# Kernel optimization log

Hardware: AMD Instinct MI355X
Metric: run time of the kernel (lower is better)

Reference implementation:

```python
import jax, jax.numpy as jnp
import numpy as np

WORLD_SIZE = 8
RANK = 3              # simulated rank; exercises a non-trivial zig-zag mask
Q_HEAD = 32
KV_HEAD = 8
HEAD_DIM = 128
SEQLEN = 8192                         # max_seqlen_q == max_seqlen_k
Q_SHARD_LEN = SEQLEN // WORLD_SIZE    # 1024 tokens per rank
CHUNK = Q_SHARD_LEN // 2              # zig-zag chunk size (512)
GROUP = Q_HEAD // KV_HEAD             # GQA group size


def _zigzag_pos(r):
    # Global token positions owned by rank r under zig-zag partitioning:
    # sequence split into 2W chunks; rank r owns chunks r and (2W-1-r).
    a = jnp.arange(CHUNK) + r * CHUNK
    b = jnp.arange(CHUNK) + (2 * WORLD_SIZE - 1 - r) * CHUNK
    return jnp.concatenate([a, b])


def setup_inputs() -> dict:
    key = jax.random.key(0)
    k1, k2, k3 = jax.random.split(key, 3)
    q_shard = jax.random.normal(k1, (Q_SHARD_LEN, Q_HEAD, HEAD_DIM), jnp.float32)
    k_shard = jax.random.normal(k2, (WORLD_SIZE, SEQLEN // WORLD_SIZE, KV_HEAD, HEAD_DIM), jnp.float32)
    v_shard = jax.random.normal(k3, (WORLD_SIZE, SEQLEN // WORLD_SIZE, KV_HEAD, HEAD_DIM), jnp.float32)
    cu_seqlens_q = jnp.array([0, Q_SHARD_LEN], dtype=jnp.int32)
    cu_seqlens_k = jnp.array([0, SEQLEN], dtype=jnp.int32)
    return {"q_shard": q_shard, "k_shard": k_shard, "v_shard": v_shard,
            "cu_seqlens_q": cu_seqlens_q, "cu_seqlens_k": cu_seqlens_k}


def reference(q_shard, k_shard, v_shard, cu_seqlens_q, cu_seqlens_k):
    # All-gather of k/v shards across ranks == concat along sequence axis.
    k = k_shard.reshape(SEQLEN, KV_HEAD, HEAD_DIM)
    v = v_shard.reshape(SEQLEN, KV_HEAD, HEAD_DIM)

    # Global positions for this rank's queries and the gathered keys
    q_pos = _zigzag_pos(RANK)                                               # [Lq]
    k_pos = jnp.concatenate([_zigzag_pos(r) for r in range(WORLD_SIZE)])    # [Sk]

    scale = 1.0 / np.sqrt(HEAD_DIM).astype(np.float32)
    qg = q_shard.reshape(Q_SHARD_LEN, KV_HEAD, GROUP, HEAD_DIM)
    # scores: [Hkv, G, Lq, Sk]
    scores = jnp.einsum('qhgd,khd->hgqk', qg, k) * scale

    # Zig-zag causal mask on GLOBAL positions
    causal = q_pos[:, None] >= k_pos[None, :]                               # [Lq, Sk]
    scores = jnp.where(causal[None, None], scores, -jnp.inf)

    p = jax.nn.softmax(scores, axis=-1)
    out = jnp.einsum('hgqk,khd->qhgd', p, v)
    return out.reshape(Q_SHARD_LEN, Q_HEAD, HEAD_DIM)
```

## Files before the change

### kernel.cpp

```cpp
#include <hip/hip_runtime.h>
#include <hip/hip_bf16.h>

typedef __bf16 bf16x8 __attribute__((ext_vector_type(8)));
typedef float  f32x4  __attribute__((ext_vector_type(4)));

#define LQ   1024
#define HQ   32
#define HKV  8
#define GRP  4
#define DH   128
#define CHK  512
#define KB   32
#define RHN  (LQ * HQ)
#define NSPLIT 4
#define QSCALE (0.08838834764831845f * 1.44269504088896341f)
#define MASKVAL (-3.0e38f)


__device__ __forceinline__ void attn_tile(
    char* __restrict__ lds, char* __restrict__ pbase,
    const float* __restrict__ kg, const float* __restrict__ vg,
    int hkv, int krow, int cbase, bool masked,
    int tid, int l16, int lhi, int qrel0,
    const bf16x8 (&qf)[4], f32x4 (&acc)[8], float (&m_r)[4], float (&l_r)[4])
{
    __syncthreads();
    {
        const int key = tid >> 3;
        const int d0  = (tid & 7) << 4;
        const float* kp = kg + ((krow + key) * HKV + hkv) * DH + d0;
        const float* vp = vg + ((krow + key) * HKV + hkv) * DH + d0;
        f32x4 a0 = *(const f32x4*)(kp);
        f32x4 a1 = *(const f32x4*)(kp + 4);
        f32x4 a2 = *(const f32x4*)(kp + 8);
        f32x4 a3 = *(const f32x4*)(kp + 12);
        bf16x8 b0, b1;
        #pragma unroll
        for (int j = 0; j < 4; ++j) {
            b0[j] = (__bf16)a0[j]; b0[j + 4] = (__bf16)a1[j];
            b1[j] = (__bf16)a2[j]; b1[j + 4] = (__bf16)a3[j];
        }
        const int kbyte = key * 256 + d0 * 2;
        const int ksw   = (key & 7) << 4;
        *(bf16x8*)(lds + ((kbyte)      ^ ksw)) = b0;
        *(bf16x8*)(lds + ((kbyte + 16) ^ ksw)) = b1;

        f32x4 c0 = *(const f32x4*)(vp);
        f32x4 c1 = *(const f32x4*)(vp + 4);
        f32x4 c2 = *(const f32x4*)(vp + 8);
        f32x4 c3 = *(const f32x4*)(vp + 12);
        #pragma unroll
        for (int i = 0; i < 16; ++i) {
            float fv = (i < 4) ? c0[i] : (i < 8) ? c1[i - 4]
                     : (i < 12) ? c2[i - 8] : c3[i - 12];
            const int d = d0 + i;
            const int vsw = ((d & 7) ^ ((d >> 4) & 7)) << 4;
            const int vbyte = (d * 64 + key * 2) ^ vsw;
            *(__bf16*)(lds + 8192 + vbyte) = (__bf16)fv;
        }
    }
    __syncthreads();

    f32x4 s0 = f32x4{0.f, 0.f, 0.f, 0.f};
    f32x4 s1 = f32x4{0.f, 0.f, 0.f, 0.f};
    __builtin_amdgcn_s_setprio(1);
    #pragma unroll
    for (int kb = 0; kb < 4; ++kb) {
        const int dby = (kb * 32 + lhi * 8) * 2;
        bf16x8 k0 = *(const bf16x8*)(lds + ((l16 * 256 + dby)        ^ ((l16 & 7) << 4)));
        bf16x8 k1 = *(const bf16x8*)(lds + (((l16 + 16) * 256 + dby) ^ ((l16 & 7) << 4)));
        s0 = __builtin_amdgcn_mfma_f32_16x16x32_bf16(qf[kb], k0, s0, 0, 0, 0);
        s1 = __builtin_amdgcn_mfma_f32_16x16x32_bf16(qf[kb], k1, s1, 0, 0, 0);
    }
    __builtin_amdgcn_s_setprio(0);

    if (masked) {
        #pragma unroll
        for (int r = 0; r < 4; ++r) {
            const int qrel = qrel0 + lhi * 4 + r;
            if (cbase + l16 > qrel)      s0[r] = MASKVAL;
            if (cbase + 16 + l16 > qrel) s1[r] = MASKVAL;
        }
    }

    float pmax[4];
    #pragma unroll
    for (int r = 0; r < 4; ++r) pmax[r] = fmaxf(s0[r], s1[r]);
    #pragma unroll
    for (int off = 1; off < 16; off <<= 1) {
        #pragma unroll
        for (int r = 0; r < 4; ++r)
            pmax[r] = fmaxf(pmax[r], __shfl_xor(pmax[r], off));
    }

    f32x4 p0, p1;
    float alpha[4], rsum[4];
    #pragma unroll
    for (int r = 0; r < 4; ++r) {
        const float mnew = fmaxf(m_r[r], pmax[r]);
        alpha[r] = exp2f(m_r[r] - mnew);
        m_r[r]   = mnew;
        p0[r] = exp2f(s0[r] - mnew);
        p1[r] = exp2f(s1[r] - mnew);
        rsum[r] = p0[r] + p1[r];
    }
    #pragma unroll
    for (int off = 1; off < 16; off <<= 1) {
        #pragma unroll
        for (int r = 0; r < 4; ++r)
            rsum[r] += __shfl_xor(rsum[r], off);
    }
    #pragma unroll
    for (int r = 0; r < 4; ++r) l_r[r] = l_r[r] * alpha[r] + rsum[r];
    #pragma unroll
    for (int nb = 0; nb < 8; ++nb) {
        #pragma unroll
        for (int r = 0; r < 4; ++r) acc[nb][r] *= alpha[r];
    }

    #pragma unroll
    for (int r = 0; r < 4; ++r) {
        const int rq  = lhi * 4 + r;
        const int rsw = (rq & 7) << 4;
        *(__bf16*)(pbase + ((rq * 64 + l16 * 2)        ^ rsw)) = (__bf16)p0[r];
        *(__bf16*)(pbase + ((rq * 64 + (l16 + 16) * 2) ^ rsw)) = (__bf16)p1[r];
    }
    bf16x8 pa = *(const bf16x8*)(pbase + ((l16 * 64 + lhi * 16) ^ ((l16 & 7) << 4)));
    __builtin_amdgcn_s_setprio(1);
    #pragma unroll
    for (int nb = 0; nb < 8; ++nb) {
        const int d = nb * 16 + l16;
        const int vsw = ((d & 7) ^ (nb & 7)) << 4;
        bf16x8 vb = *(const bf16x8*)(lds + 8192 + ((d * 64 + lhi * 16) ^ vsw));
        acc[nb] = __builtin_amdgcn_mfma_f32_16x16x32_bf16(pa, vb, acc[nb], 0, 0, 0);
    }
    __builtin_amdgcn_s_setprio(0);
}

__device__ __forceinline__ void load_qfrag(const float* __restrict__ qg,
                                           int qr0, int h, int l16, int lhi,
                                           bf16x8 (&qf)[4])
{
    const float* qp = qg + ((qr0 + l16) * HQ + h) * DH + lhi * 8;
    #pragma unroll
    for (int kb = 0; kb < 4; ++kb) {
        f32x4 t0 = *(const f32x4*)(qp + kb * 32);
        f32x4 t1 = *(const f32x4*)(qp + kb * 32 + 4);
        bf16x8 f;
        #pragma unroll
        for (int j = 0; j < 4; ++j) {
            f[j]     = (__bf16)(t0[j] * QSCALE);
            f[j + 4] = (__bf16)(t1[j] * QSCALE);
        }
        qf[kb] = f;
    }
}

__global__ __launch_bounds__(256, 2)
void zz_attn_part(const float* __restrict__ qg, const float* __restrict__ kg,
                  const float* __restrict__ vg,
                  float* __restrict__ Op, float* __restrict__ mp, float* __restrict__ lp)
{
    __shared__ __align__(16) char lds[20480];
    const int bid = blockIdx.x;
    int half, part, q_tile, hkv;
    if (bid < 256) { half = 0; part = 0; q_tile = bid & 31;              hkv = bid >> 5; }
    else { const int e = bid - 256; half = 1; part = e & 3;
           q_tile = 32 + ((e >> 2) & 31);                                hkv = e >> 7; }

    const int tid  = threadIdx.x;
    const int w    = tid >> 6;
    const int lane = tid & 63;
    const int l16  = lane & 15;
    const int lhi  = lane >> 4;
    const int h    = hkv * GRP + w;
    const int qr0  = q_tile << 4;
    const int qrel0 = (q_tile & 31) << 4;

    bf16x8 qf[4];
    load_qfrag(qg, qr0, h, l16, lhi, qf);

    f32x4 acc[8];
    #pragma unroll
    for (int i = 0; i < 8; ++i) acc[i] = f32x4{0.f, 0.f, 0.f, 0.f};
    float m_r[4], l_r[4];
    #pragma unroll
    for (int r = 0; r < 4; ++r) { m_r[r] = -1e30f; l_r[r] = 0.f; }

    char* const pbase = lds + 16384 + w * 1024;

    unsigned fullmask;
    int diag_slot;
    if (half == 0) { fullmask = 0x0015u; diag_slot = 6; }
    else {
        fullmask = (part == 0) ? 0x0015u : (part == 1) ? 0x0340u
                 : (part == 2) ? 0x1C00u : 0xE000u;
        diag_slot = (part == 3) ? 7 : -1;
    }

    #pragma unroll 1
    for (int s = 0; s < 16; ++s) {
        if (!((fullmask >> s) & 1)) continue;
        #pragma unroll 1
        for (int t = 0; t < 16; ++t)
            attn_tile(lds, pbase, kg, vg, hkv, s * CHK + t * KB, 0, false,
                      tid, l16, lhi, qrel0, qf, acc, m_r, l_r);
    }
    if (diag_slot >= 0) {
        const int nd = (qrel0 >> 5) + 1;
        #pragma unroll 1
        for (int t = 0; t < nd; ++t)
            attn_tile(lds, pbase, kg, vg, hkv, diag_slot * CHK + t * KB, t * KB, true,
                      tid, l16, lhi, qrel0, qf, acc, m_r, l_r);
    }

    float* op = Op + (size_t)part * (LQ * HQ * DH) + ((qr0 + lhi * 4) * HQ + h) * DH + l16;
    #pragma unroll
    for (int nb = 0; nb < 8; ++nb) {
        #pragma unroll
        for (int r = 0; r < 4; ++r)
            op[r * (HQ * DH) + nb * 16] = acc[nb][r];
    }
    if (l16 == 0) {
        #pragma unroll
        for (int r = 0; r < 4; ++r) {
            const int rh = (qr0 + lhi * 4 + r) * HQ + h;
            mp[part * RHN + rh] = m_r[r];
            lp[part * RHN + rh] = l_r[r];
            if (half == 0) {
                #pragma unroll
                for (int s = 1; s < NSPLIT; ++s) {
                    mp[s * RHN + rh] = -1e30f;
                    lp[s * RHN + rh] = 0.f;
                }
            }
        }
    }
}

__global__ __launch_bounds__(256)
void zz_combine(const float* __restrict__ Op, const float* __restrict__ mp,
                const float* __restrict__ lp, float* __restrict__ outg)
{
    const int flat = blockIdx.x * 256 + threadIdx.x;
    const int rh = flat >> 5;
    const int d4 = (flat & 31) << 2;
    const float m0 = mp[rh], m1 = mp[RHN + rh], m2 = mp[2 * RHN + rh], m3 = mp[3 * RHN + rh];
    const float M  = fmaxf(fmaxf(m0, m1), fmaxf(m2, m3));
    const float w0 = exp2f(m0 - M), w1 = exp2f(m1 - M), w2 = exp2f(m2 - M), w3 = exp2f(m3 - M);
    const float den = w0 * lp[rh] + w1 * lp[RHN + rh] + w2 * lp[2 * RHN + rh] + w3 * lp[3 * RHN + rh];
    const size_t base = (size_t)rh * DH + d4;
    f32x4 a0 = *(const f32x4*)(Op + base);
    f32x4 a1 = *(const f32x4*)(Op + (size_t)LQ * HQ * DH + base);
    f32x4 a2 = *(const f32x4*)(Op + (size_t)2 * LQ * HQ * DH + base);
    f32x4 a3 = *(const f32x4*)(Op + (size_t)3 * LQ * HQ * DH + base);
    f32x4 num = w0 * a0 + w1 * a1 + w2 * a2 + w3 * a3;
    const float inv = 1.0f / den;
    *(f32x4*)(outg + base) = num * inv;
}

__global__ __launch_bounds__(256, 2)
void zz_attn_mono(const float* __restrict__ qg, const float* __restrict__ kg,
                  const float* __restrict__ vg, float* __restrict__ outg)
{
    __shared__ __align__(16) char lds[20480];
    const int bid    = blockIdx.x;
    const int q_tile = bid & 63;
    const int hkv    = bid >> 6;
    const int tid    = threadIdx.x;
    const int w      = tid >> 6;
    const int lane   = tid & 63;
    const int l16    = lane & 15;
    const int lhi    = lane >> 4;
    const int h      = hkv * GRP + w;
    const int qr0    = q_tile << 4;
    const int half   = q_tile >> 5;
    const int qrel0  = (q_tile & 31) << 4;

    bf16x8 qf[4];
    load_qfrag(qg, qr0, h, l16, lhi, qf);

    f32x4 acc[8];
    #pragma unroll
    for (int i = 0; i < 8; ++i) acc[i] = f32x4{0.f, 0.f, 0.f, 0.f};
    float m_r[4], l_r[4];
    #pragma unroll
    for (int r = 0; r < 4; ++r) { m_r[r] = -1e30f; l_r[r] = 0.f; }

    char* const pbase = lds + 16384 + w * 1024;

    const unsigned int fullmask = half ? 0xFF55u : 0x0015u;
    const int diag_slot = half ? 7 : 6;

    #pragma unroll 1
    for (int s = 0; s < 16; ++s) {
        if (!((fullmask >> s) & 1)) continue;
        #pragma unroll 1
        for (int t = 0; t < 16; ++t)
            attn_tile(lds, pbase, kg, vg, hkv, s * CHK + t * KB, 0, false,
                      tid, l16, lhi, qrel0, qf, acc, m_r, l_r);
    }
    const int nd = (qrel0 >> 5) + 1;
    #pragma unroll 1
    for (int t = 0; t < nd; ++t)
        attn_tile(lds, pbase, kg, vg, hkv, diag_slot * CHK + t * KB, t * KB, true,
                  tid, l16, lhi, qrel0, qf, acc, m_r, l_r);

    #pragma unroll
    for (int r = 0; r < 4; ++r) l_r[r] = 1.0f / l_r[r];
    float* op = outg + (qr0 + lhi * 4) * (HQ * DH) + h * DH + l16;
    #pragma unroll
    for (int nb = 0; nb < 8; ++nb) {
        #pragma unroll
        for (int r = 0; r < 4; ++r)
            op[r * (HQ * DH) + nb * 16] = acc[nb][r] * l_r[r];
    }
}

extern "C" void kernel_launch(void* const* d_in, const int* in_sizes, int n_in,
                              void* d_out, int out_size, void* d_ws, size_t ws_size,
                              hipStream_t stream)
{
    (void)in_sizes; (void)n_in; (void)out_size;
    const float* q = (const float*)d_in[0];
    const float* k = (const float*)d_in[1];
    const float* v = (const float*)d_in[2];
    float* out = (float*)d_out;

    const size_t need = (size_t)NSPLIT * LQ * HQ * DH * 4
                      + (size_t)2 * NSPLIT * RHN * 4;
    if (ws_size >= need) {
        float* Op = (float*)d_ws;
        float* mp = Op + (size_t)NSPLIT * LQ * HQ * DH;
        float* lp = mp + (size_t)NSPLIT * RHN;
        hipLaunchKernelGGL(zz_attn_part, dim3(1280), dim3(256), 0, stream, q, k, v, Op, mp, lp);
        hipLaunchKernelGGL(zz_combine, dim3((RHN * DH / 4) / 256), dim3(256), 0, stream,
                           Op, mp, lp, out);
    } else {
        hipLaunchKernelGGL(zz_attn_mono, dim3(512), dim3(256), 0, stream, q, k, v, out);
    }
}
```

Baseline: 448.9 us.

## Pre-convert K/V to bf16 tiles and double-buffer with async global-to-LDS loads

Adds a prep kernel that converts K and V once into bf16, pre-swizzled and pre-transposed tiles in workspace. The main kernel then streams those tiles straight into a double-buffered LDS with global_load_lds, so the next tile loads while the current one computes, and it drops the per-tile fp32-to-bf16 conversion and scattered V stores. It also reorders the block index so heads are interleaved and raises occupancy to 4 blocks per CU. The cost is an extra kernel launch, an extra pass over K/V memory, and more LDS per block. The fallback path now also requires the split workspace.

```diff
diff --git a/kernel.cpp b/kernel.cpp
--- a/kernel.cpp
+++ b/kernel.cpp
@@ -13,129 +13,14 @@
 #define KB   32
 #define RHN  (LQ * HQ)
 #define NSPLIT 4
+#define TILE_BYTES 8192
+#define HKV_BYTES  (256 * TILE_BYTES)
 #define QSCALE (0.08838834764831845f * 1.44269504088896341f)
 #define MASKVAL (-3.0e38f)
 
-
-__device__ __forceinline__ void attn_tile(
-    char* __restrict__ lds, char* __restrict__ pbase,
-    const float* __restrict__ kg, const float* __restrict__ vg,
-    int hkv, int krow, int cbase, bool masked,
-    int tid, int l16, int lhi, int qrel0,
-    const bf16x8 (&qf)[4], f32x4 (&acc)[8], float (&m_r)[4], float (&l_r)[4])
-{
-    __syncthreads();
-    {
-        const int key = tid >> 3;
-        const int d0  = (tid & 7) << 4;
-        const float* kp = kg + ((krow + key) * HKV + hkv) * DH + d0;
-        const float* vp = vg + ((krow + key) * HKV + hkv) * DH + d0;
-        f32x4 a0 = *(const f32x4*)(kp);
-        f32x4 a1 = *(const f32x4*)(kp + 4);
-        f32x4 a2 = *(const f32x4*)(kp + 8);
-        f32x4 a3 = *(const f32x4*)(kp + 12);
-        bf16x8 b0, b1;
-        #pragma unroll
-        for (int j = 0; j < 4; ++j) {
-            b0[j] = (__bf16)a0[j]; b0[j + 4] = (__bf16)a1[j];
-            b1[j] = (__bf16)a2[j]; b1[j + 4] = (__bf16)a3[j];
-        }
-        const int kbyte = key * 256 + d0 * 2;
-        const int ksw   = (key & 7) << 4;
-        *(bf16x8*)(lds + ((kbyte)      ^ ksw)) = b0;
-        *(bf16x8*)(lds + ((kbyte + 16) ^ ksw)) = b1;
-
-        f32x4 c0 = *(const f32x4*)(vp);
-        f32x4 c1 = *(const f32x4*)(vp + 4);
-        f32x4 c2 = *(const f32x4*)(vp + 8);
-        f32x4 c3 = *(const f32x4*)(vp + 12);
-        #pragma unroll
-        for (int i = 0; i < 16; ++i) {
-            float fv = (i < 4) ? c0[i] : (i < 8) ? c1[i - 4]
-                     : (i < 12) ? c2[i - 8] : c3[i - 12];
-            const int d = d0 + i;
-            const int vsw = ((d & 7) ^ ((d >> 4) & 7)) << 4;
-            const int vbyte = (d * 64 + key * 2) ^ vsw;
-            *(__bf16*)(lds + 8192 + vbyte) = (__bf16)fv;
-        }
-    }
-    __syncthreads();
-
-    f32x4 s0 = f32x4{0.f, 0.f, 0.f, 0.f};
-    f32x4 s1 = f32x4{0.f, 0.f, 0.f, 0.f};
-    __builtin_amdgcn_s_setprio(1);
-    #pragma unroll
-    for (int kb = 0; kb < 4; ++kb) {
-        const int dby = (kb * 32 + lhi * 8) * 2;
-        bf16x8 k0 = *(const bf16x8*)(lds + ((l16 * 256 + dby)        ^ ((l16 & 7) << 4)));
-        bf16x8 k1 = *(const bf16x8*)(lds + (((l16 + 16) * 256 + dby) ^ ((l16 & 7) << 4)));
-        s0 = __builtin_amdgcn_mfma_f32_16x16x32_bf16(qf[kb], k0, s0, 0, 0, 0);
-        s1 = __builtin_amdgcn_mfma_f32_16x16x32_bf16(qf[kb], k1, s1, 0, 0, 0);
-    }
-    __builtin_amdgcn_s_setprio(0);
-
-    if (masked) {
-        #pragma unroll
-        for (int r = 0; r < 4; ++r) {
-            const int qrel = qrel0 + lhi * 4 + r;
-            if (cbase + l16 > qrel)      s0[r] = MASKVAL;
-            if (cbase + 16 + l16 > qrel) s1[r] = MASKVAL;
-        }
-    }
-
-    float pmax[4];
-    #pragma unroll
-    for (int r = 0; r < 4; ++r) pmax[r] = fmaxf(s0[r], s1[r]);
-    #pragma unroll
-    for (int off = 1; off < 16; off <<= 1) {
-        #pragma unroll
-        for (int r = 0; r < 4; ++r)
-            pmax[r] = fmaxf(pmax[r], __shfl_xor(pmax[r], off));
-    }
-
-    f32x4 p0, p1;
-    float alpha[4], rsum[4];
-    #pragma unroll
-    for (int r = 0; r < 4; ++r) {
-        const float mnew = fmaxf(m_r[r], pmax[r]);
-        alpha[r] = exp2f(m_r[r] - mnew);
-        m_r[r]   = mnew;
-        p0[r] = exp2f(s0[r] - mnew);
-        p1[r] = exp2f(s1[r] - mnew);
-        rsum[r] = p0[r] + p1[r];
-    }
-    #pragma unroll
-    for (int off = 1; off < 16; off <<= 1) {
-        #pragma unroll
-        for (int r = 0; r < 4; ++r)
-            rsum[r] += __shfl_xor(rsum[r], off);
-    }
-    #pragma unroll
-    for (int r = 0; r < 4; ++r) l_r[r] = l_r[r] * alpha[r] + rsum[r];
-    #pragma unroll
-    for (int nb = 0; nb < 8; ++nb) {
-        #pragma unroll
-        for (int r = 0; r < 4; ++r) acc[nb][r] *= alpha[r];
-    }
-
-    #pragma unroll
-    for (int r = 0; r < 4; ++r) {
-        const int rq  = lhi * 4 + r;
-        const int rsw = (rq & 7) << 4;
-        *(__bf16*)(pbase + ((rq * 64 + l16 * 2)        ^ rsw)) = (__bf16)p0[r];
-        *(__bf16*)(pbase + ((rq * 64 + (l16 + 16) * 2) ^ rsw)) = (__bf16)p1[r];
-    }
-    bf16x8 pa = *(const bf16x8*)(pbase + ((l16 * 64 + lhi * 16) ^ ((l16 & 7) << 4)));
-    __builtin_amdgcn_s_setprio(1);
-    #pragma unroll
-    for (int nb = 0; nb < 8; ++nb) {
-        const int d = nb * 16 + l16;
-        const int vsw = ((d & 7) ^ (nb & 7)) << 4;
-        bf16x8 vb = *(const bf16x8*)(lds + 8192 + ((d * 64 + lhi * 16) ^ vsw));
-        acc[nb] = __builtin_amdgcn_mfma_f32_16x16x32_bf16(pa, vb, acc[nb], 0, 0, 0);
-    }
-    __builtin_amdgcn_s_setprio(0);
-}
+typedef __attribute__((address_space(1))) const void gvoid_t;
+typedef __attribute__((address_space(3))) void lvoid_t;
+#define GLL(g, l) __builtin_amdgcn_global_load_lds((gvoid_t*)(g), (lvoid_t*)(l), 16, 0, 0)
 
 __device__ __forceinline__ void load_qfrag(const float* __restrict__ qg,
                                            int qr0, int h, int l16, int lhi,
@@ -156,17 +41,55 @@
     }
 }
 
-__global__ __launch_bounds__(256, 2)
-void zz_attn_part(const float* __restrict__ qg, const float* __restrict__ kg,
-                  const float* __restrict__ vg,
-                  float* __restrict__ Op, float* __restrict__ mp, float* __restrict__ lp)
-{
-    __shared__ __align__(16) char lds[20480];
+__global__ __launch_bounds__(256)
+void zz_prep(const float* __restrict__ kg, const float* __restrict__ vg,
+             char* __restrict__ Kp, char* __restrict__ Vp)
+{
+    const int bid  = blockIdx.x;
+    const int hkv  = bid & 7;
+    const int tile = bid >> 3;
+    const int tid  = threadIdx.x;
+    char* ko = Kp + (size_t)hkv * HKV_BYTES + (size_t)tile * TILE_BYTES;
+    char* vo = Vp + (size_t)hkv * HKV_BYTES + (size_t)tile * TILE_BYTES;
+
+    #pragma unroll
+    for (int p = 0; p < 2; ++p) {
+        const int gid = tid + p * 256;
+        const int key = gid >> 4;
+        const int dbg = gid & 15;
+        const float* src = kg + ((size_t)(tile * 32 + key) * HKV + hkv) * DH + dbg * 8;
+        f32x4 t0 = *(const f32x4*)src;
+        f32x4 t1 = *(const f32x4*)(src + 4);
+        bf16x8 b;
+        #pragma unroll
+        for (int j = 0; j < 4; ++j) { b[j] = (__bf16)t0[j]; b[j + 4] = (__bf16)t1[j]; }
+        *(bf16x8*)(ko + key * 256 + ((dbg * 16) ^ ((key & 7) << 4))) = b;
+    }
+    #pragma unroll
+    for (int p = 0; p < 2; ++p) {
+        const int gid = tid + p * 256;
+        const int d   = gid & 127;
+        const int kg2 = (tid >> 7) + p * 2;
+        bf16x8 b;
+        #pragma unroll
+        for (int j = 0; j < 8; ++j)
+            b[j] = (__bf16)vg[((size_t)(tile * 32 + kg2 * 8 + j) * HKV + hkv) * DH + d];
+        *(bf16x8*)(vo + kg2 * 2048 + d * 16) = b;
+    }
+}
+
+__global__ __launch_bounds__(256, 4)
+void zz_part2(const float* __restrict__ qg, const char* __restrict__ Kp,
+              const char* __restrict__ Vp,
+              float* __restrict__ Op, float* __restrict__ mp, float* __restrict__ lp)
+{
+    __shared__ __align__(16) char lds[36864];
     const int bid = blockIdx.x;
-    int half, part, q_tile, hkv;
-    if (bid < 256) { half = 0; part = 0; q_tile = bid & 31;              hkv = bid >> 5; }
-    else { const int e = bid - 256; half = 1; part = e & 3;
-           q_tile = 32 + ((e >> 2) & 31);                                hkv = e >> 7; }
+    const int hkv = bid & 7;
+    const int e   = bid >> 3;
+    int half, part, q_tile;
+    if (e < 32) { half = 0; part = 0; q_tile = e; }
+    else { half = 1; part = (e - 32) >> 5; q_tile = 32 + ((e - 32) & 31); }
 
     const int tid  = threadIdx.x;
     const int w    = tid >> 6;
@@ -187,31 +110,129 @@
     #pragma unroll
     for (int r = 0; r < 4; ++r) { m_r[r] = -1e30f; l_r[r] = 0.f; }
 
-    char* const pbase = lds + 16384 + w * 1024;
-
-    unsigned fullmask;
-    int diag_slot;
+    char* const pbase = lds + 32768 + w * 1024;
+
+    unsigned fullmask; int diag_slot;
     if (half == 0) { fullmask = 0x0015u; diag_slot = 6; }
     else {
         fullmask = (part == 0) ? 0x0015u : (part == 1) ? 0x0340u
                  : (part == 2) ? 0x1C00u : 0xE000u;
         diag_slot = (part == 3) ? 7 : -1;
     }
-
-    #pragma unroll 1
-    for (int s = 0; s < 16; ++s) {
-        if (!((fullmask >> s) & 1)) continue;
-        #pragma unroll 1
-        for (int t = 0; t < 16; ++t)
-            attn_tile(lds, pbase, kg, vg, hkv, s * CHK + t * KB, 0, false,
-                      tid, l16, lhi, qrel0, qf, acc, m_r, l_r);
-    }
-    if (diag_slot >= 0) {
-        const int nd = (qrel0 >> 5) + 1;
-        #pragma unroll 1
-        for (int t = 0; t < nd; ++t)
-            attn_tile(lds, pbase, kg, vg, hkv, diag_slot * CHK + t * KB, t * KB, true,
-                      tid, l16, lhi, qrel0, qf, acc, m_r, l_r);
+    const int nd = (diag_slot >= 0) ? ((qrel0 >> 5) + 1) : 0;
+
+    const char* kpg = Kp + (size_t)hkv * HKV_BYTES + w * 2048 + lane * 16;
+    const char* vpg = Vp + (size_t)hkv * HKV_BYTES + w * 2048 + lane * 16;
+
+    auto stage = [&](int gt, int b) {
+        const char* kt = kpg + (size_t)gt * TILE_BYTES;
+        const char* vt = vpg + (size_t)gt * TILE_BYTES;
+        char* kd = lds + b * 16384 + w * 2048;
+        GLL(kt, kd); GLL(kt + 1024, kd + 1024);
+        char* vd = kd + 8192;
+        GLL(vt, vd); GLL(vt + 1024, vd + 1024);
+    };
+    auto gt_of = [&](unsigned rem, int t) {
+        return rem ? ((int)(__builtin_ctz(rem) << 4) + t) : (diag_slot * 16 + t);
+    };
+    auto adv = [](unsigned& rem, int& t) {
+        ++t; if (rem && t == 16) { rem &= rem - 1; t = 0; }
+    };
+
+    const int ksw16 = (l16 & 7) << 4;
+    const int vlane = lhi * 2048 + l16 * 16;
+
+    unsigned remC = fullmask; int tC = 0;
+    unsigned remN = remC;     int tN = 0; adv(remN, tN);
+    stage(gt_of(remC, tC), 0);
+    __syncthreads();
+    int cur = 0;
+
+    while (true) {
+        const bool nv = (remN != 0) || (tN < nd);
+        if (nv) stage(gt_of(remN, tN), cur ^ 1);
+
+        char* kb_ = lds + cur * 16384;
+        char* vb_ = kb_ + 8192;
+        const bool masked = (remC == 0);
+        const int  cbase  = masked ? (tC << 5) : 0;
+
+        f32x4 s0 = f32x4{0.f, 0.f, 0.f, 0.f};
+        f32x4 s1 = f32x4{0.f, 0.f, 0.f, 0.f};
+        __builtin_amdgcn_s_setprio(1);
+        #pragma unroll
+        for (int kb = 0; kb < 4; ++kb) {
+            const int dby = kb * 64 + lhi * 16;
+            bf16x8 k0 = *(const bf16x8*)(kb_ + ((l16 * 256 + dby)        ^ ksw16));
+            bf16x8 k1 = *(const bf16x8*)(kb_ + (((l16 + 16) * 256 + dby) ^ ksw16));
+            s0 = __builtin_amdgcn_mfma_f32_16x16x32_bf16(qf[kb], k0, s0, 0, 0, 0);
+            s1 = __builtin_amdgcn_mfma_f32_16x16x32_bf16(qf[kb], k1, s1, 0, 0, 0);
+        }
+        __builtin_amdgcn_s_setprio(0);
+
+        if (masked) {
+            #pragma unroll
+            for (int r = 0; r < 4; ++r) {
+                const int qrel = qrel0 + lhi * 4 + r;
+                if (cbase + l16 > qrel)      s0[r] = MASKVAL;
+                if (cbase + 16 + l16 > qrel) s1[r] = MASKVAL;
+            }
+        }
+
+        float pmax[4];
+        #pragma unroll
+        for (int r = 0; r < 4; ++r) pmax[r] = fmaxf(s0[r], s1[r]);
+        #pragma unroll
+        for (int off = 1; off < 16; off <<= 1) {
+            #pragma unroll
+            for (int r = 0; r < 4; ++r)
+                pmax[r] = fmaxf(pmax[r], __shfl_xor(pmax[r], off));
+        }
+
+        f32x4 p0, p1;
+        float alpha[4], rsum[4];
+        #pragma unroll
+        for (int r = 0; r < 4; ++r) {
+            const float mnew = fmaxf(m_r[r], pmax[r]);
+            alpha[r] = exp2f(m_r[r] - mnew);
+            m_r[r]   = mnew;
+            p0[r] = exp2f(s0[r] - mnew);
+            p1[r] = exp2f(s1[r] - mnew);
+            rsum[r] = p0[r] + p1[r];
+        }
+        #pragma unroll
+        for (int off = 1; off < 16; off <<= 1) {
+            #pragma unroll
+            for (int r = 0; r < 4; ++r)
+                rsum[r] += __shfl_xor(rsum[r], off);
+        }
+        #pragma unroll
+        for (int r = 0; r < 4; ++r) l_r[r] = l_r[r] * alpha[r] + rsum[r];
+        #pragma unroll
+        for (int nb = 0; nb < 8; ++nb) {
+            #pragma unroll
+            for (int r = 0; r < 4; ++r) acc[nb][r] *= alpha[r];
+        }
+
+        #pragma unroll
+        for (int r = 0; r < 4; ++r) {
+            const int rq  = lhi * 4 + r;
+            const int rsw = (rq & 7) << 4;
+            *(__bf16*)(pbase + ((rq * 64 + l16 * 2)        ^ rsw)) = (__bf16)p0[r];
+            *(__bf16*)(pbase + ((rq * 64 + (l16 + 16) * 2) ^ rsw)) = (__bf16)p1[r];
+        }
+        bf16x8 pa = *(const bf16x8*)(pbase + ((l16 * 64 + lhi * 16) ^ ksw16));
+        __builtin_amdgcn_s_setprio(1);
+        #pragma unroll
+        for (int nb = 0; nb < 8; ++nb) {
+            bf16x8 vb = *(const bf16x8*)(vb_ + vlane + nb * 256);
+            acc[nb] = __builtin_amdgcn_mfma_f32_16x16x32_bf16(pa, vb, acc[nb], 0, 0, 0);
+        }
+        __builtin_amdgcn_s_setprio(0);
+
+        __syncthreads();
+        if (!nv) break;
+        cur ^= 1; remC = remN; tC = tN; adv(remN, tN);
     }
 
     float* op = Op + (size_t)part * (LQ * HQ * DH) + ((qr0 + lhi * 4) * HQ + h) * DH + l16;
@@ -259,61 +280,191 @@
     *(f32x4*)(outg + base) = num * inv;
 }
 
+__device__ __forceinline__ void attn_tile_f32(
+    char* __restrict__ lds, char* __restrict__ pbase,
+    const float* __restrict__ kg, const float* __restrict__ vg,
+    int hkv, int krow, int cbase, bool masked,
+    int tid, int l16, int lhi, int qrel0,
+    const bf16x8 (&qf)[4], f32x4 (&acc)[8], float (&m_r)[4], float (&l_r)[4])
+{
+    __syncthreads();
+    {
+        const int key = tid >> 3;
+        const int d0  = (tid & 7) << 4;
+        const float* kp = kg + ((krow + key) * HKV + hkv) * DH + d0;
+        const float* vp = vg + ((krow + key) * HKV + hkv) * DH + d0;
+        f32x4 a0 = *(const f32x4*)(kp);
+        f32x4 a1 = *(const f32x4*)(kp + 4);
+        f32x4 a2 = *(const f32x4*)(kp + 8);
+        f32x4 a3 = *(const f32x4*)(kp + 12);
+        bf16x8 b0, b1;
+        #pragma unroll
+        for (int j = 0; j < 4; ++j) {
+            b0[j] = (__bf16)a0[j]; b0[j + 4] = (__bf16)a1[j];
+            b1[j] = (__bf16)a2[j]; b1[j + 4] = (__bf16)a3[j];
+        }
+        const int kbyte = key * 256 + d0 * 2;
+        const int ksw   = (key & 7) << 4;
+        *(bf16x8*)(lds + ((kbyte)      ^ ksw)) = b0;
+        *(bf16x8*)(lds + ((kbyte + 16) ^ ksw)) = b1;
+
+        f32x4 c0 = *(const f32x4*)(vp);
+        f32x4 c1 = *(const f32x4*)(vp + 4);
+        f32x4 c2 = *(const f32x4*)(vp + 8);
+        f32x4 c3 = *(const f32x4*)(vp + 12);
+        #pragma unroll
+        for (int i = 0; i < 16; ++i) {
+            float fv = (i < 4) ? c0[i] : (i < 8) ? c1[i - 4]
+                     : (i < 12) ? c2[i - 8] : c3[i - 12];
+            const int d = d0 + i;
+            const int vsw = ((d & 7) ^ ((d >> 4) & 7)) << 4;
+            const int vbyte = (d * 64 + key * 2) ^ vsw;
+            *(__bf16*)(lds + 8192 + vbyte) = (__bf16)fv;
+        }
+    }
+    __syncthreads();
+
+    f32x4 s0 = f32x4{0.f, 0.f, 0.f, 0.f};
+    f32x4 s1 = f32x4{0.f, 0.f, 0.f, 0.f};
+    #pragma unroll
+    for (int kb = 0; kb < 4; ++kb) {
+        const int dby = (kb * 32 + lhi * 8) * 2;
+        bf16x8 k0 = *(const bf16x8*)(lds + ((l16 * 256 + dby)        ^ ((l16 & 7) << 4)));
+        bf16x8 k1 = *(const bf16x8*)(lds + (((l16 + 16) * 256 + dby) ^ ((l16 & 7) << 4)));
+        s0 = __builtin_amdgcn_mfma_f32_16x16x32_bf16(qf[kb], k0, s0, 0, 0, 0);
+        s1 = __builtin_amdgcn_mfma_f32_16x16x32_bf16(qf[kb], k1, s1, 0, 0, 0);
+    }
+    if (masked) {
+        #pragma unroll
+        for (int r = 0; r < 4; ++r) {
+            const int qrel = qrel0 + lhi * 4 + r;
+            if (cbase + l16 > qrel)      s0[r] = MASKVAL;
+            if (cbase + 16 + l16 > qrel) s1[r] = MASKVAL;
+        }
+    }
+    float pmax[4];
+    #pragma unroll
+    for (int r = 0; r < 4; ++r) pmax[r] = fmaxf(s0[r], s1[r]);
+    #pragma unroll
+    for (int off = 1; off < 16; off <<= 1) {
+        #pragma unroll
+        for (int r = 0; r < 4; ++r)
+            pmax[r] = fmaxf(pmax[r], __shfl_xor(pmax[r], off));
+    }
+    f32x4 p0, p1;
+    float alpha[4], rsum[4];
+    #pragma unroll
+    for (int r = 0; r < 4; ++r) {
+        const float mnew = fmaxf(m_r[r], pmax[r]);
+        alpha[r] = exp2f(m_r[r] - mnew);
+        m_r[r]   = mnew;
+        p0[r] = exp2f(s0[r] - mnew);
+        p1[r] = exp2f(s1[r] - mnew);
+        rsum[r] = p0[r] + p1[r];
+    }
+    #pragma unroll
+    for (int off = 1; off < 16; off <<= 1) {
+        #pragma unroll
+        for (int r = 0; r < 4; ++r)
+            rsum[r] += __shfl_xor(rsum[r], off);
+    }
+    #pragma unroll
+    for (int r = 0; r < 4; ++r) l_r[r] = l_r[r] * alpha[r] + rsum[r];
+    #pragma unroll
+    for (int nb = 0; nb < 8; ++nb) {
+        #pragma unroll
+        for (int r = 0; r < 4; ++r) acc[nb][r] *= alpha[r];
+    }
+    #pragma unroll
+    for (int r = 0; r < 4; ++r) {
+        const int rq  = lhi * 4 + r;
+        const int rsw = (rq & 7) << 4;
+        *(__bf16*)(pbase + ((rq * 64 + l16 * 2)        ^ rsw)) = (__bf16)p0[r];
+        *(__bf16*)(pbase + ((rq * 64 + (l16 + 16) * 2) ^ rsw)) = (__bf16)p1[r];
+    }
+    bf16x8 pa = *(const bf16x8*)(pbase + ((l16 * 64 + lhi * 16) ^ ((l16 & 7) << 4)));
+    #pragma unroll
+    for (int nb = 0; nb < 8; ++nb) {
+        const int d = nb * 16 + l16;
+        const int vsw = ((d & 7) ^ (nb & 7)) << 4;
+        bf16x8 vb = *(const bf16x8*)(lds + 8192 + ((d * 64 + lhi * 16) ^ vsw));
+        acc[nb] = __builtin_amdgcn_mfma_f32_16x16x32_bf16(pa, vb, acc[nb], 0, 0, 0);
+    }
+}
+
 __global__ __launch_bounds__(256, 2)
-void zz_attn_mono(const float* __restrict__ qg, const float* __restrict__ kg,
-                  const float* __restrict__ vg, float* __restrict__ outg)
+void zz_attn_part_old(const float* __restrict__ qg, const float* __restrict__ kg,
+                      const float* __restrict__ vg,
+                      float* __restrict__ Op, float* __restrict__ mp, float* __restrict__ lp)
 {
     __shared__ __align__(16) char lds[20480];
-    const int bid    = blockIdx.x;
-    const int q_tile = bid & 63;
-    const int hkv    = bid >> 6;
-    const int tid    = threadIdx.x;
-    const int w      = tid >> 6;
-    const int lane   = tid & 63;
-    const int l16    = lane & 15;
-    const int lhi    = lane >> 4;
-    const int h      = hkv * GRP + w;
-    const int qr0    = q_tile << 4;
-    const int half   = q_tile >> 5;
-    const int qrel0  = (q_tile & 31) << 4;
+    const int bid = blockIdx.x;
+    int half, part, q_tile, hkv;
+    if (bid < 256) { half = 0; part = 0; q_tile = bid & 31; hkv = bid >> 5; }
+    else { const int e = bid - 256; half = 1; part = e & 3;
+           q_tile = 32 + ((e >> 2) & 31); hkv = e >> 7; }
+    const int tid  = threadIdx.x;
+    const int w    = tid >> 6;
+    const int lane = tid & 63;
+    const int l16  = lane & 15;
+    const int lhi  = lane >> 4;
+    const int h    = hkv * GRP + w;
+    const int qr0  = q_tile << 4;
+    const int qrel0 = (q_tile & 31) << 4;
 
     bf16x8 qf[4];
     load_qfrag(qg, qr0, h, l16, lhi, qf);
-
     f32x4 acc[8];
     #pragma unroll
     for (int i = 0; i < 8; ++i) acc[i] = f32x4{0.f, 0.f, 0.f, 0.f};
     float m_r[4], l_r[4];
     #pragma unroll
     for (int r = 0; r < 4; ++r) { m_r[r] = -1e30f; l_r[r] = 0.f; }
-
     char* const pbase = lds + 16384 + w * 1024;
 
-    const unsigned int fullmask = half ? 0xFF55u : 0x0015u;
-    const int diag_slot = half ? 7 : 6;
-
+    unsigned fullmask; int diag_slot;
+    if (half == 0) { fullmask = 0x0015u; diag_slot = 6; }
+    else {
+        fullmask = (part == 0) ? 0x0015u : (part == 1) ? 0x0340u
+                 : (part == 2) ? 0x1C00u : 0xE000u;
+        diag_slot = (part == 3) ? 7 : -1;
+    }
     #pragma unroll 1
     for (int s = 0; s < 16; ++s) {
         if (!((fullmask >> s) & 1)) continue;
         #pragma unroll 1
         for (int t = 0; t < 16; ++t)
-            attn_tile(lds, pbase, kg, vg, hkv, s * CHK + t * KB, 0, false,
-                      tid, l16, lhi, qrel0, qf, acc, m_r, l_r);
-    }
-    const int nd = (qrel0 >> 5) + 1;
-    #pragma unroll 1
-    for (int t = 0; t < nd; ++t)
-        attn_tile(lds, pbase, kg, vg, hkv, diag_slot * CHK + t * KB, t * KB, true,
-                  tid, l16, lhi, qrel0, qf, acc, m_r, l_r);
-
-    #pragma unroll
-    for (int r = 0; r < 4; ++r) l_r[r] = 1.0f / l_r[r];
-    float* op = outg + (qr0 + lhi * 4) * (HQ * DH) + h * DH + l16;
+            attn_tile_f32(lds, pbase, kg, vg, hkv, s * CHK + t * KB, 0, false,
+                          tid, l16, lhi, qrel0, qf, acc, m_r, l_r);
+    }
+    if (diag_slot >= 0) {
+        const int nd = (qrel0 >> 5) + 1;
+        #pragma unroll 1
+        for (int t = 0; t < nd; ++t)
+            attn_tile_f32(lds, pbase, kg, vg, hkv, diag_slot * CHK + t * KB, t * KB, true,
+                          tid, l16, lhi, qrel0, qf, acc, m_r, l_r);
+    }
+    float* op = Op + (size_t)part * (LQ * HQ * DH) + ((qr0 + lhi * 4) * HQ + h) * DH + l16;
     #pragma unroll
     for (int nb = 0; nb < 8; ++nb) {
         #pragma unroll
         for (int r = 0; r < 4; ++r)
-            op[r * (HQ * DH) + nb * 16] = acc[nb][r] * l_r[r];
+            op[r * (HQ * DH) + nb * 16] = acc[nb][r];
+    }
+    if (l16 == 0) {
+        #pragma unroll
+        for (int r = 0; r < 4; ++r) {
+            const int rh = (qr0 + lhi * 4 + r) * HQ + h;
+            mp[part * RHN + rh] = m_r[r];
+            lp[part * RHN + rh] = l_r[r];
+            if (half == 0) {
+                #pragma unroll
+                for (int s = 1; s < NSPLIT; ++s) {
+                    mp[s * RHN + rh] = -1e30f;
+                    lp[s * RHN + rh] = 0.f;
+                }
+            }
+        }
     }
 }
 
@@ -327,16 +478,26 @@
     const float* v = (const float*)d_in[2];
     float* out = (float*)d_out;
 
-    const size_t need = (size_t)NSPLIT * LQ * HQ * DH * 4
-                      + (size_t)2 * NSPLIT * RHN * 4;
-    if (ws_size >= need) {
-        float* Op = (float*)d_ws;
-        float* mp = Op + (size_t)NSPLIT * LQ * HQ * DH;
-        float* lp = mp + (size_t)NSPLIT * RHN;
-        hipLaunchKernelGGL(zz_attn_part, dim3(1280), dim3(256), 0, stream, q, k, v, Op, mp, lp);
+    const size_t sz_op = (size_t)NSPLIT * LQ * HQ * DH * 4;
+    const size_t sz_ml = (size_t)NSPLIT * RHN * 4;
+    const size_t sz_kv = (size_t)HKV * HKV_BYTES;
+    const size_t need_split = sz_op + 2 * sz_ml;
+    const size_t need_full  = need_split + 2 * sz_kv;
+
+    float* Op = (float*)d_ws;
+    float* mp = (float*)((char*)d_ws + sz_op);
+    float* lp = (float*)((char*)d_ws + sz_op + sz_ml);
+
+    if (ws_size >= need_full) {
+        char* Kp = (char*)d_ws + need_split;
+        char* Vp = Kp + sz_kv;
+        hipLaunchKernelGGL(zz_prep,  dim3(2048), dim3(256), 0, stream, k, v, Kp, Vp);
+        hipLaunchKernelGGL(zz_part2, dim3(1280), dim3(256), 0, stream, q, Kp, Vp, Op, mp, lp);
         hipLaunchKernelGGL(zz_combine, dim3((RHN * DH / 4) / 256), dim3(256), 0, stream,
                            Op, mp, lp, out);
     } else {
-        hipLaunchKernelGGL(zz_attn_mono, dim3(512), dim3(256), 0, stream, q, k, v, out);
-    }
-}
+        hipLaunchKernelGGL(zz_attn_part_old, dim3(1280), dim3(256), 0, stream, q, k, v, Op, mp, lp);
+        hipLaunchKernelGGL(zz_combine, dim3((RHN * DH / 4) / 256), dim3(256), 0, stream,
+                           Op, mp, lp, out);
+    }
+}
```

New measurement: 383.9 us. -14.5%, faster.
